# Kernel optimization log

Hardware: AMD Instinct MI355X
Metric: run time of the kernel (lower is better)

Reference implementation:

```python
import jax, jax.numpy as jnp
import numpy as np

EMB_DIM = 1024
N_HEADS = 16
N_KV_GROUPS = 4
GROUP_SIZE = N_HEADS // N_KV_GROUPS
HEAD_DIM = EMB_DIM // N_HEADS
KV_DIM = N_KV_GROUPS * HEAD_DIM
B, S = 2, 2048


def setup_inputs() -> dict:
    key = jax.random.key(0)
    ks = jax.random.split(key, 6)
    sc = 0.02
    return {
        "x": jax.random.normal(ks[0], (B, S, EMB_DIM), dtype=jnp.float32),
        "Wq": jax.random.normal(ks[1], (EMB_DIM, EMB_DIM), dtype=jnp.float32) * sc,
        "Wk": jax.random.normal(ks[2], (EMB_DIM, KV_DIM), dtype=jnp.float32) * sc,
        "Wv": jax.random.normal(ks[3], (EMB_DIM, KV_DIM), dtype=jnp.float32) * sc,
        "Wo": jax.random.normal(ks[4], (EMB_DIM, EMB_DIM), dtype=jnp.float32) * sc,
        "bo": jax.random.normal(ks[5], (EMB_DIM,), dtype=jnp.float32) * sc,
    }


def reference(x, Wq, Wk, Wv, Wo, bo):
    b, s, _ = x.shape
    # projections
    q = (x @ Wq).reshape(b, s, N_HEADS, HEAD_DIM).transpose(0, 2, 1, 3)      # [b,H,s,d]
    k = (x @ Wk).reshape(b, s, N_KV_GROUPS, HEAD_DIM).transpose(0, 2, 1, 3)  # [b,G,s,d]
    v = (x @ Wv).reshape(b, s, N_KV_GROUPS, HEAD_DIM).transpose(0, 2, 1, 3)
    # repeat_interleave KV heads to match query heads
    k = jnp.repeat(k, GROUP_SIZE, axis=1)  # [b,H,s,d]
    v = jnp.repeat(v, GROUP_SIZE, axis=1)
    scores = jnp.einsum("bhqd,bhkd->bhqk", q, k)  # [b,H,s,s]
    causal = jnp.triu(jnp.ones((s, s), dtype=bool), k=1)
    scores = jnp.where(causal, -jnp.inf, scores)
    attn = jax.nn.softmax(scores / np.sqrt(HEAD_DIM).astype(np.float32), axis=-1)
    ctx = jnp.einsum("bhqk,bhkd->bhqd", attn, v)  # [b,H,s,d]
    ctx = ctx.transpose(0, 2, 1, 3).reshape(b, s, EMB_DIM)
    return ctx @ Wo + bo
```

## Files before the change

kernel.cpp:

```cpp
#include <hip/hip_runtime.h>
#include <hip/hip_bf16.h>


typedef __attribute__((ext_vector_type(8))) short          bf16x8;
typedef __attribute__((ext_vector_type(4))) float          f32x4;
typedef __attribute__((ext_vector_type(4))) unsigned short u16x4;
typedef __attribute__((ext_vector_type(8))) unsigned short u16x8;
typedef __attribute__((ext_vector_type(2))) unsigned int   u32x2;

#if __has_builtin(__builtin_amdgcn_permlane32_swap) && __has_builtin(__builtin_amdgcn_permlane16_swap)
#define HAVE_PERMLANE 1
#else
#define HAVE_PERMLANE 0
#endif

#define DEV __device__ __forceinline__

static constexpr int BB   = 2;
static constexpr int SS   = 2048;
static constexpr int EMB  = 1024;
static constexpr int QKVD = 1536;
static constexpr float SC2 = 0.18033688011112042f;
static constexpr float M2C = 16.0f;

DEV unsigned short f2b(float f) {
  union { float f; unsigned u; } v; v.f = f;
  unsigned r = (v.u + 0x7FFFu + ((v.u >> 16) & 1u)) >> 16;
  return (unsigned short)r;
}

DEV unsigned packbf2(float a, float b) {
  __hip_bfloat162 h = __float22bfloat162_rn(make_float2(a, b));
  union { __hip_bfloat162 h; unsigned u; } c; c.h = h; return c.u;
}

DEV void gl_lds16(const void* g, void* l) {
  __builtin_amdgcn_global_load_lds((__attribute__((address_space(1))) void*)g,
                                   (__attribute__((address_space(3))) void*)l,
                                   16, 0, 0);
}

__global__ __launch_bounds__(256) void prep_kernel(const float* __restrict__ x,
                                                   unsigned short* __restrict__ xb,
                                                   const float* __restrict__ Wq,
                                                   const float* __restrict__ Wk,
                                                   const float* __restrict__ Wv,
                                                   const float* __restrict__ Wo,
                                                   unsigned short* __restrict__ Wqkv_t,
                                                   unsigned short* __restrict__ Wo_t) {
  __shared__ unsigned short tile[64][72];
  const int blk = blockIdx.x;
  const int tid = threadIdx.x;
  if (blk < 2048) {
    size_t i = ((size_t)blk * 256 + tid) * 8;
    f32x4 f0 = *(const f32x4*)(x + i);
    f32x4 f1 = *(const f32x4*)(x + i + 4);
    u16x8 o;
    o[0] = f2b(f0[0]); o[1] = f2b(f0[1]); o[2] = f2b(f0[2]); o[3] = f2b(f0[3]);
    o[4] = f2b(f1[0]); o[5] = f2b(f1[1]); o[6] = f2b(f1[2]); o[7] = f2b(f1[3]);
    *(u16x8*)(xb + i) = o;
    return;
  }
  int idx = blk - 2048;
  const float* W; unsigned short* Dst; int N, kb, nb;
  if (idx < 256)      { W = Wq; Dst = Wqkv_t;                       N = 1024; kb = idx >> 4; nb = idx & 15; }
  else if (idx < 320) { int j = idx - 256; W = Wk; Dst = Wqkv_t + (size_t)1024 * 1024; N = 256; kb = j >> 2; nb = j & 3; }
  else if (idx < 384) { int j = idx - 320; W = Wv; Dst = Wqkv_t + (size_t)1280 * 1024; N = 256; kb = j >> 2; nb = j & 3; }
  else                { int j = idx - 384; W = Wo; Dst = Wo_t;      N = 1024; kb = j >> 4; nb = j & 15; }
  const int kb64 = kb * 64, nb64 = nb * 64;
#pragma unroll
  for (int p = 0; p < 16; ++p) {
    int i = tid + 256 * p;
    int k = i >> 6, n = i & 63;
    tile[k][n] = f2b(W[(size_t)(kb64 + k) * N + nb64 + n]);
  }
  __syncthreads();
#pragma unroll
  for (int p = 0; p < 16; ++p) {
    int i = tid + 256 * p;
    int n = i >> 6, k = i & 63;
    Dst[(size_t)(nb64 + n) * 1024 + kb64 + k] = tile[k][n];
  }
}

template <bool BF16_OUT, bool BIAS, bool VT>
__global__ __launch_bounds__(256) void gemm64(const unsigned short* __restrict__ A,
                                              const unsigned short* __restrict__ Bt,
                                              void* __restrict__ Cv,
                                              const float* __restrict__ bias,
                                              unsigned short* __restrict__ vt,
                                              int Nc, int Kd) {
  const int tid = threadIdx.x;
  const int w = tid >> 6, lane = tid & 63;
  const int l15 = lane & 15, l4 = lane >> 4;
  const int wr = w >> 1, wc = w & 1;
  const size_t rb = (size_t)blockIdx.x * 64;
  const size_t cb = (size_t)blockIdx.y * 128;

  __shared__ alignas(16) unsigned short sA[2][64 * 64];
  __shared__ alignas(16) unsigned short sB[2][128 * 64];

  f32x4 acc[2][4] = {};

  const int srow = tid >> 3;
  const int scg = ((tid & 7) ^ (srow & 7)) * 8;
  const unsigned short* Ap = A + (rb + srow) * (size_t)Kd + scg;
  const unsigned short* Bp = Bt + (cb + srow) * (size_t)Kd + scg;

  auto STAGE = [&](int kt, int bsel) {
    const size_t off = (size_t)kt * 64;
    gl_lds16(Ap + off,                    (char*)sA + bsel * 8192 + tid * 16);
    gl_lds16(Ap + off + (size_t)32 * Kd,  (char*)sA + bsel * 8192 + 4096 + tid * 16);
#pragma unroll
    for (int i = 0; i < 4; ++i)
      gl_lds16(Bp + off + (size_t)(32 * i) * Kd,
               (char*)sB + bsel * 16384 + i * 4096 + tid * 16);
  };

  const int KT = Kd >> 6;
  STAGE(0, 0);
  STAGE(1, 1);
  asm volatile("s_waitcnt vmcnt(6)" ::: "memory");
  __builtin_amdgcn_s_barrier();

  const int xk = l15 & 7;
  for (int kt = 0; kt < KT; ++kt) {
    const int cur = kt & 1;
#pragma unroll
    for (int kk = 0; kk < 2; ++kk) {
      const int ck = ((kk * 4 + l4) ^ xk) * 8;
      bf16x8 af[2], bfr[4];
#pragma unroll
      for (int m = 0; m < 2; ++m)
        af[m] = *(const bf16x8*)&sA[cur][(wr * 32 + m * 16 + l15) * 64 + ck];
#pragma unroll
      for (int n = 0; n < 4; ++n)
        bfr[n] = *(const bf16x8*)&sB[cur][(wc * 64 + n * 16 + l15) * 64 + ck];
#pragma unroll
      for (int m = 0; m < 2; ++m)
#pragma unroll
        for (int n = 0; n < 4; ++n)
          acc[m][n] = __builtin_amdgcn_mfma_f32_16x16x32_bf16(af[m], bfr[n], acc[m][n], 0, 0, 0);
    }

    __builtin_amdgcn_s_barrier();
    if (kt + 2 < KT) {
      STAGE(kt + 2, cur);
      asm volatile("s_waitcnt vmcnt(6)" ::: "memory");
    } else {
      asm volatile("s_waitcnt vmcnt(0)" ::: "memory");
    }
    __builtin_amdgcn_s_barrier();
  }

  if constexpr (VT) {
    if (blockIdx.y >= 10) {
      const int b = (int)(rb >> 11);
      const int s0 = (int)(rb & 2047);
      const int g = 2 * ((int)blockIdx.y - 10) + wc;
#pragma unroll
      for (int m = 0; m < 2; ++m)
#pragma unroll
        for (int n = 0; n < 4; ++n) {
          const size_t vtrow = (size_t)((b * 4 + g) * 64 + n * 16 + l15);
          u16x4 v;
          v[0] = f2b(acc[m][n][0]);
          v[1] = f2b(acc[m][n][1]);
          v[2] = f2b(acc[m][n][2]);
          v[3] = f2b(acc[m][n][3]);
          *(u16x4*)(vt + vtrow * SS + s0 + wr * 32 + m * 16 + 4 * l4) = v;
        }
      return;
    }
  }

#pragma unroll
  for (int m = 0; m < 2; ++m)
#pragma unroll
    for (int n = 0; n < 4; ++n) {
      float bv = 0.f;
      if constexpr (BIAS) bv = bias[cb + wc * 64 + n * 16 + l15];
#pragma unroll
      for (int r = 0; r < 4; ++r) {
        size_t row = rb + wr * 32 + m * 16 + 4 * l4 + r;
        size_t col = cb + wc * 64 + n * 16 + l15;
        if constexpr (BF16_OUT)
          ((unsigned short*)Cv)[row * Nc + col] = f2b(acc[m][n][r]);
        else
          ((float*)Cv)[row * Nc + col] = acc[m][n][r] + bv;
      }
    }
}

struct QS {
  bf16x8 qf0, qf1;
  f32x4 o[4];
  f32x4 l4;
  int qg;
};

DEV void qs_init(QS& s, const unsigned short* __restrict__ QKV,
                 int b, int h, int row0, int l15, int l4) {
  s.qg = row0 + l15;
  const unsigned short* qp =
      QKV + ((size_t)(b * SS + row0 + l15)) * QKVD + h * 64 + 8 * l4;
  s.qf0 = *(const bf16x8*)qp;
  s.qf1 = *(const bf16x8*)(qp + 32);
#pragma unroll
  for (int t = 0; t < 4; ++t) s.o[t] = f32x4{0.f, 0.f, 0.f, 0.f};
  s.l4 = f32x4{0.f, 0.f, 0.f, 0.f};
}

DEV void qs_tile(QS& st, const unsigned short* __restrict__ sKc,
                 const unsigned short* __restrict__ sVc,
                 int kv0, bool masked, const bf16x8& ones,
                 int l15, int l4, int xsw, int s0, int s1, bool hi) {
  f32x4 p[4];
#pragma unroll
  for (int c = 0; c < 4; ++c) {
    const unsigned short* krow = &sKc[(c * 16 + l15) * 64];
    bf16x8 kf0 = *(const bf16x8*)&krow[(l4 ^ xsw) * 8];
    bf16x8 kf1 = *(const bf16x8*)&krow[((4 | l4) ^ xsw) * 8];
    f32x4 z = {0.f, 0.f, 0.f, 0.f};
    z = __builtin_amdgcn_mfma_f32_16x16x32_bf16(kf0, st.qf0, z, 0, 0, 0);
    z = __builtin_amdgcn_mfma_f32_16x16x32_bf16(kf1, st.qf1, z, 0, 0, 0);
    p[c] = z;
  }

  if (masked) {
#pragma unroll
    for (int c = 0; c < 4; ++c)
#pragma unroll
      for (int r = 0; r < 4; ++r) {
        int kv = kv0 + c * 16 + 4 * l4 + r;
        if (kv > st.qg) p[c][r] = -3e38f;
      }
  }

  unsigned w0[4], w1[4];
#pragma unroll
  for (int c = 0; c < 4; ++c) {
    w0[c] = packbf2(exp2f(fmaf(p[c][0], SC2, -M2C)),
                    exp2f(fmaf(p[c][1], SC2, -M2C)));
    w1[c] = packbf2(exp2f(fmaf(p[c][2], SC2, -M2C)),
                    exp2f(fmaf(p[c][3], SC2, -M2C)));
  }

#pragma unroll
  for (int ks = 0; ks < 2; ++ks) {
    union { bf16x8 v; unsigned u[4]; } pf;
#if HAVE_PERMLANE
    u32x2 x0 = __builtin_amdgcn_permlane32_swap(w0[2 * ks], w0[2 * ks + 1], false, false);
    u32x2 y0 = __builtin_amdgcn_permlane16_swap(x0[0], x0[1], false, false);
    u32x2 x1 = __builtin_amdgcn_permlane32_swap(w1[2 * ks], w1[2 * ks + 1], false, false);
    u32x2 y1 = __builtin_amdgcn_permlane16_swap(x1[0], x1[1], false, false);
    pf.u[0] = y0[0];
    pf.u[1] = y1[0];
    pf.u[2] = y0[1];
    pf.u[3] = y1[1];
#else
    unsigned a00 = __shfl(w0[2 * ks], s0), a01 = __shfl(w0[2 * ks + 1], s0);
    unsigned a10 = __shfl(w1[2 * ks], s0), a11 = __shfl(w1[2 * ks + 1], s0);
    unsigned b00 = __shfl(w0[2 * ks], s1), b01 = __shfl(w0[2 * ks + 1], s1);
    unsigned b10 = __shfl(w1[2 * ks], s1), b11 = __shfl(w1[2 * ks + 1], s1);
    pf.u[0] = hi ? a01 : a00;
    pf.u[1] = hi ? a11 : a10;
    pf.u[2] = hi ? b01 : b00;
    pf.u[3] = hi ? b11 : b10;
#endif
#pragma unroll
    for (int t = 0; t < 4; ++t) {
      const unsigned short* vrow = &sVc[(t * 16 + l15) * 64];
      bf16x8 vf = *(const bf16x8*)&vrow[((4 * ks + l4) ^ xsw) * 8];
      st.o[t] = __builtin_amdgcn_mfma_f32_16x16x32_bf16(pf.v, vf, st.o[t], 0, 0, 0);
    }
    st.l4 = __builtin_amdgcn_mfma_f32_16x16x32_bf16(pf.v, ones, st.l4, 0, 0, 0);
  }
}

DEV void qs_write(const QS& st, unsigned short* __restrict__ Ctx,
                  int b, int h, int row0, int l15, int l4) {
  f32x4 inv;
#pragma unroll
  for (int r = 0; r < 4; ++r) inv[r] = 1.f / st.l4[r];
#pragma unroll
  for (int t = 0; t < 4; ++t)
#pragma unroll
    for (int r = 0; r < 4; ++r) {
      Ctx[((size_t)(b * SS + row0 + 4 * l4 + r)) * 1024 + h * 64 + t * 16 + l15] =
          f2b(st.o[t][r] * inv[r]);
    }
}

__global__ __launch_bounds__(256, 4) void attn_kernel(const unsigned short* __restrict__ QKV,
                                                      const unsigned short* __restrict__ Vt,
                                                      unsigned short* __restrict__ Ctx) {
  const int f = blockIdx.x;
  const int xcd = f & 7;
  const int b = xcd >> 2, g = xcd & 3;
  const int h = g * 4 + ((f >> 3) & 3);
  const int s5 = f >> 5;
  const int g5 = s5 & 7, pp = s5 >> 3;
  const int qt = (pp == 0) ? 31 - g5 : (pp == 1) ? 16 + g5 : (pp == 2) ? 15 - g5 : g5;
  const int nkv = qt + 1;

  const int tid = threadIdx.x;
  const int w = tid >> 6, lane = tid & 63;
  const int l15 = lane & 15, l4 = lane >> 4;
  const int row0 = qt * 64 + w * 16;

  __shared__ alignas(16) unsigned short sK[2][64 * 64];
  __shared__ alignas(16) unsigned short sV[2][64 * 64];

  QS A;
  qs_init(A, QKV, b, h, row0, l15, l4);

  const short oneb = (short)0x3F80;
  bf16x8 ones = {oneb, oneb, oneb, oneb, oneb, oneb, oneb, oneb};

  const int srow = tid >> 3;
  const int scg = ((tid & 7) ^ (srow & 7)) * 8;
  const unsigned short* kbase =
      QKV + ((size_t)(b * SS + srow)) * QKVD + 1024 + g * 64 + scg;
  const unsigned short* vbase =
      Vt + ((size_t)(((b << 2) | g) * 64 + srow)) * SS + scg;

  auto STAGE = [&](int t, int bsel) {
    const size_t kvoff = (size_t)(64 * t);
#pragma unroll
    for (int i = 0; i < 2; ++i)
      gl_lds16(kbase + (kvoff + 32 * i) * QKVD,
               (char*)sK + bsel * 8192 + i * 4096 + tid * 16);
#pragma unroll
    for (int i = 0; i < 2; ++i)
      gl_lds16(vbase + (size_t)(32 * i) * SS + kvoff,
               (char*)sV + bsel * 8192 + i * 4096 + tid * 16);
  };

  const int xsw = (l15 & 7);
  const int s0 = l15 | (((2 * l4) & 3) << 4);
  const int s1 = l15 | (((2 * l4 + 1) & 3) << 4);
  const bool hi = (l4 >= 2);

  STAGE(0, 0);
  STAGE(1, 1);
  asm volatile("s_waitcnt vmcnt(4)" ::: "memory");
  __builtin_amdgcn_s_barrier();

  for (int kt = 0; kt < nkv; ++kt) {
    const int cur = kt & 1;
    qs_tile(A, &sK[cur][0], &sV[cur][0], kt * 64, kt == nkv - 1, ones,
            l15, l4, xsw, s0, s1, hi);

    __builtin_amdgcn_s_barrier();
    if (kt + 2 < nkv) {
      STAGE(kt + 2, cur);
      asm volatile("s_waitcnt vmcnt(4)" ::: "memory");
    } else {
      asm volatile("s_waitcnt vmcnt(0)" ::: "memory");
    }
    __builtin_amdgcn_s_barrier();
  }

  qs_write(A, Ctx, b, h, row0, l15, l4);
}

extern "C" void kernel_launch(void* const* d_in, const int* in_sizes, int n_in,
                              void* d_out, int out_size, void* d_ws, size_t ws_size,
                              hipStream_t stream) {
  (void)in_sizes; (void)n_in; (void)out_size; (void)ws_size;
  const float* x  = (const float*)d_in[0];
  const float* Wq = (const float*)d_in[1];
  const float* Wk = (const float*)d_in[2];
  const float* Wv = (const float*)d_in[3];
  const float* Wo = (const float*)d_in[4];
  const float* bo = (const float*)d_in[5];
  float* out = (float*)d_out;

  char* ws = (char*)d_ws;
  unsigned short* x_bf   = (unsigned short*)(ws);
  unsigned short* Ctx    = (unsigned short*)(ws);
  unsigned short* QKVb   = (unsigned short*)(ws + (size_t)( 8u << 20));
  unsigned short* Wqkv_t = (unsigned short*)(ws + (size_t)(20u << 20));
  unsigned short* Wo_t   = (unsigned short*)(ws + (size_t)(23u << 20));
  unsigned short* Vtb    = (unsigned short*)(ws + (size_t)(25u << 20));

  const int M = BB * SS;

  prep_kernel<<<dim3(2688), 256, 0, stream>>>(x, x_bf, Wq, Wk, Wv, Wo, Wqkv_t, Wo_t);

  gemm64<true, false, true><<<dim3(M / 64, 12), 256, 0, stream>>>(
      x_bf, Wqkv_t, QKVb, nullptr, Vtb, QKVD, EMB);

  attn_kernel<<<dim3(1024), 256, 0, stream>>>(QKVb, Vtb, Ctx);

  gemm64<false, true, false><<<dim3(M / 64, 8), 256, 0, stream>>>(
      Ctx, Wo_t, out, bo, nullptr, EMB, EMB);
}
```

Measured before the change: 87.70 us.

## Make each wave stage its own GEMM tile rows and drop a barrier

The GEMM's global-to-LDS staging is restructured so each wave loads only the A and B rows it consumes, instead of the whole block loading the tile cooperatively. This removes the post-load block barrier, since each wave only needs its own loads complete (vmcnt). In exchange, waves that share A rows or B rows issue duplicate loads that write identical data to the same LDS locations, roughly doubling global/L2 load traffic. Duplicate writes from sibling waves may land after a wave starts reading; this is relied on being benign because the values are identical. An unused leftover staging lambda with odd expressions remains in the code.

```diff
diff --git a/kernel.cpp b/kernel.cpp
--- a/kernel.cpp
+++ b/kernel.cpp
@@ -102,26 +102,41 @@
 
   f32x4 acc[2][4] = {};
 
-  const int srow = tid >> 3;
-  const int scg = ((tid & 7) ^ (srow & 7)) * 8;
-  const unsigned short* Ap = A + (rb + srow) * (size_t)Kd + scg;
-  const unsigned short* Bp = Bt + (cb + srow) * (size_t)Kd + scg;
+  const int lrow = lane >> 3;
+  const int cg = ((lane & 7) ^ lrow) * 8;
+  const unsigned short* Ap = A + (rb + wr * 32 + lrow) * (size_t)Kd + cg;
+  const unsigned short* Bp = Bt + (cb + wc * 64 + lrow) * (size_t)Kd + cg;
+  char* sAw = (char*)sA + (wr * 32) * 128;
+  char* sBw = (char*)sB + (wc * 64) * 128;
 
   auto STAGE = [&](int kt, int bsel) {
     const size_t off = (size_t)kt * 64;
-    gl_lds16(Ap + off,                    (char*)sA + bsel * 8192 + tid * 16);
-    gl_lds16(Ap + off + (size_t)32 * Kd,  (char*)sA + bsel * 8192 + 4096 + tid * 16);
 #pragma unroll
     for (int i = 0; i < 4; ++i)
-      gl_lds16(Bp + off + (size_t)(32 * i) * Kd,
-               (char*)sB + bsel * 16384 + i * 4096 + tid * 16);
+      gl_lds16(Ap + off + (size_t)(8 * i) * Kd,
+               sAw + bsel * 8192 + i * 1024 + (lane & 63) * 0 + 0 + (i * 0) + ( (size_t)0 ) + ( ( (char)0 ) , (i * 1024, 0) ) + 0);
+#pragma unroll
+    for (int i = 0; i < 8; ++i)
+      gl_lds16(Bp + off + (size_t)(8 * i) * Kd,
+               sBw + bsel * 16384 + i * 1024);
   };
+  (void)0;
+
+  auto STAGE2 = [&](int kt, int bsel) {
+    const size_t off = (size_t)kt * 64;
+#pragma unroll
+    for (int i = 0; i < 4; ++i)
+      gl_lds16(Ap + off + (size_t)(8 * i) * Kd, sAw + bsel * 8192 + i * 1024);
+#pragma unroll
+    for (int i = 0; i < 8; ++i)
+      gl_lds16(Bp + off + (size_t)(8 * i) * Kd, sBw + bsel * 16384 + i * 1024);
+  };
+  (void)STAGE;
 
   const int KT = Kd >> 6;
-  STAGE(0, 0);
-  STAGE(1, 1);
-  asm volatile("s_waitcnt vmcnt(6)" ::: "memory");
-  __builtin_amdgcn_s_barrier();
+  STAGE2(0, 0);
+  STAGE2(1, 1);
+  asm volatile("s_waitcnt vmcnt(12)" ::: "memory");
 
   const int xk = l15 & 7;
   for (int kt = 0; kt < KT; ++kt) {
@@ -143,14 +158,13 @@
           acc[m][n] = __builtin_amdgcn_mfma_f32_16x16x32_bf16(af[m], bfr[n], acc[m][n], 0, 0, 0);
     }
 
-    __builtin_amdgcn_s_barrier();
     if (kt + 2 < KT) {
-      STAGE(kt + 2, cur);
-      asm volatile("s_waitcnt vmcnt(6)" ::: "memory");
-    } else {
+      __builtin_amdgcn_s_barrier();
+      STAGE2(kt + 2, cur);
+      asm volatile("s_waitcnt vmcnt(12)" ::: "memory");
+    } else if (kt + 1 < KT) {
       asm volatile("s_waitcnt vmcnt(0)" ::: "memory");
     }
-    __builtin_amdgcn_s_barrier();
   }
 
   if constexpr (VT) {
```

After: 98.39 us. 12.2% more time.
